# Performance work log

Measured on AMD Instinct MI355X. Metric: run time of the kernel, lower is better.

Reference implementation:

```python
import jax, jax.numpy as jnp
import numpy as np

N = 50000
E = 800000
D_IN = 256
D_HID = 256
D_OUT = 256
EPS = 1e-5


def _sage_conv(x, src, dst, Wl, Wr, b, n_nodes):
    # mean aggregation of source-node features at target nodes (PyG SAGEConv default)
    msg = x[src]                                              # [E, d_in]
    agg = jax.ops.segment_sum(msg, dst, num_segments=n_nodes)  # [N, d_in]
    deg = jax.ops.segment_sum(jnp.ones((src.shape[0],), x.dtype), dst,
                              num_segments=n_nodes)           # [N]
    agg = agg / jnp.maximum(deg, 1.0)[:, None]
    return agg @ Wl + x @ Wr + b


def _bn(h, gamma, beta, mean, var):
    # inference-mode BatchNorm1d
    return (h - mean) * jax.lax.rsqrt(var + EPS) * gamma + beta


def setup_inputs() -> dict:
    key = jax.random.key(0)
    ks = jax.random.split(key, 16)
    x = jax.random.normal(ks[0], (N, D_IN), dtype=jnp.float32)
    edge_index = jax.random.randint(ks[1], (2, E), 0, N, dtype=jnp.int32)

    def lin(k, din, dout):
        return jax.random.normal(k, (din, dout), dtype=jnp.float32) / np.sqrt(din)

    inp = {"x": x, "edge_index": edge_index}
    dims = [(D_IN, D_HID), (D_HID, D_HID), (D_HID, D_OUT)]
    ki = 2
    for i, (din, dout) in enumerate(dims):
        inp[f"Wl{i}"] = lin(ks[ki], din, dout); ki += 1
        inp[f"Wr{i}"] = lin(ks[ki], din, dout); ki += 1
        inp[f"b{i}"] = jnp.zeros((dout,), jnp.float32)
    for i in range(2):
        inp[f"gamma{i}"] = jnp.ones((D_HID,), jnp.float32)
        inp[f"beta{i}"] = jnp.zeros((D_HID,), jnp.float32)
        inp[f"mean{i}"] = jax.random.normal(ks[ki], (D_HID,), jnp.float32) * 0.1; ki += 1
        inp[f"var{i}"] = jnp.ones((D_HID,), jnp.float32) + 0.1 * jax.random.uniform(ks[ki], (D_HID,)); ki += 1
    return inp


def reference(x, edge_index, Wl0, Wr0, b0, Wl1, Wr1, b1, Wl2, Wr2, b2,
              gamma0, beta0, mean0, var0, gamma1, beta1, mean1, var1):
    src, dst = edge_index[0], edge_index[1]
    h = x
    layers = [(Wl0, Wr0, b0, gamma0, beta0, mean0, var0),
              (Wl1, Wr1, b1, gamma1, beta1, mean1, var1)]
    for Wl, Wr, b, g, bt, m, v in layers:
        h_res = h
        h = _sage_conv(h, src, dst, Wl, Wr, b, N)
        h = jax.nn.relu(_bn(h, g, bt, m, v))
        # dropout is identity in eval mode
        if h_res.shape[1] == h.shape[1]:
            h = h + h_res
    return _sage_conv(h, src, dst, Wl2, Wr2, b2, N)
```

## Files before the change

### kernel.cpp

```cpp
#include <hip/hip_runtime.h>
#include <hip/hip_bf16.h>

#define NN 50000
#define NE 800000
#define DD 256
#define EPSV 1e-5f

typedef float f32x4 __attribute__((ext_vector_type(4)));
typedef short bf16x8s __attribute__((ext_vector_type(8)));
typedef unsigned int uint32;

__device__ __forceinline__ float lo16f(uint32 u) {
  return __builtin_bit_cast(float, u << 16);
}
__device__ __forceinline__ float hi16f(uint32 u) {
  return __builtin_bit_cast(float, u & 0xffff0000u);
}
__device__ __forceinline__ float bf2f(unsigned int u16v) {
  return __builtin_bit_cast(float, u16v << 16);
}
__device__ __forceinline__ unsigned short f2bf(float f) {
  return __builtin_bit_cast(unsigned short, __float2bfloat16(f));
}
__device__ __forceinline__ void mfma_bf16(bf16x8s a, bf16x8s b, f32x4& c) {
  asm("v_mfma_f32_16x16x32_bf16 %0, %1, %2, %0" : "+v"(c) : "v"(a), "v"(b));
}
__device__ __forceinline__ void gload_lds16(const void* g, void* l) {
  __builtin_amdgcn_global_load_lds((const __attribute__((address_space(1))) void*)g,
                                   (__attribute__((address_space(3))) void*)l, 16, 0, 0);
}



__global__ void deg_count_k(const int* __restrict__ ei, int* __restrict__ deg) {
  int e = blockIdx.x * 256 + threadIdx.x;
  if (e < NE) atomicAdd(&deg[ei[NE + e]], 1);
}

__global__ void scan1_k(const int* __restrict__ deg, int* __restrict__ row_ptr,
                        int* __restrict__ blockSums) {
  __shared__ int s[1024];
  int gid = blockIdx.x * 1024 + threadIdx.x;
  int v = (gid < NN) ? deg[gid] : 0;
  s[threadIdx.x] = v;
  __syncthreads();
  for (int off = 1; off < 1024; off <<= 1) {
    int t = (threadIdx.x >= off) ? s[threadIdx.x - off] : 0;
    __syncthreads();
    s[threadIdx.x] += t;
    __syncthreads();
  }
  if (gid < NN) row_ptr[gid] = s[threadIdx.x] - v;
  if (threadIdx.x == 1023) blockSums[blockIdx.x] = s[1023];
}

__global__ void scan2_k(const int* __restrict__ blockSums, int* __restrict__ blockOffs,
                        int* __restrict__ row_ptr, int nblocks) {
  if (threadIdx.x == 0) {
    int run = 0;
    for (int i = 0; i < nblocks; ++i) { blockOffs[i] = run; run += blockSums[i]; }
    row_ptr[NN] = run;
  }
}

__global__ void scan3_k(int* __restrict__ row_ptr, const int* __restrict__ blockOffs,
                        const int* __restrict__ deg, float* __restrict__ deg_inv) {
  int gid = blockIdx.x * 1024 + threadIdx.x;
  if (gid < NN) {
    row_ptr[gid] += blockOffs[blockIdx.x];
    deg_inv[gid] = 1.0f / (float)max(deg[gid], 1);
  }
}

__global__ void csr_fill_k(const int* __restrict__ ei, int* __restrict__ cursor,
                           unsigned short* __restrict__ col16) {
  int e = blockIdx.x * 256 + threadIdx.x;
  if (e < NE) {
    int pos = atomicAdd(&cursor[ei[NE + e]], 1);
    col16[pos] = (unsigned short)ei[e];
  }
}


__global__ __launch_bounds__(256) void split_x_k(const float* __restrict__ x,
                                                 uint32* __restrict__ xc) {
  int ni = threadIdx.x & 15, c = threadIdx.x >> 4;
  int node = blockIdx.x * 16 + ni;
  const float4* xr = reinterpret_cast<const float4*>(x + (size_t)node * DD + c * 16);
  float f[16];
#pragma unroll
  for (int qq = 0; qq < 4; ++qq) {
    float4 v = xr[qq];
    f[qq * 4 + 0] = v.x; f[qq * 4 + 1] = v.y; f[qq * 4 + 2] = v.z; f[qq * 4 + 3] = v.w;
  }
  uint32 wbuf[16];
#pragma unroll
  for (int g = 0; g < 8; ++g) {
    unsigned short h0 = f2bf(f[2 * g]), h1 = f2bf(f[2 * g + 1]);
    unsigned short l0 = f2bf(f[2 * g] - bf2f(h0));
    unsigned short l1 = f2bf(f[2 * g + 1] - bf2f(h1));
    wbuf[g] = (uint32)h0 | ((uint32)h1 << 16);
    wbuf[8 + g] = (uint32)l0 | ((uint32)l1 << 16);
  }
  uint32* dst = xc + ((size_t)c * NN + node) * 16;
#pragma unroll
  for (int qq = 0; qq < 4; ++qq)
    reinterpret_cast<uint4*>(dst)[qq] =
        make_uint4(wbuf[qq * 4], wbuf[qq * 4 + 1], wbuf[qq * 4 + 2], wbuf[qq * 4 + 3]);
}


__global__ __launch_bounds__(256) void wtprep_k(
    const float* __restrict__ W0, const float* __restrict__ W1,
    const float* __restrict__ W2, const float* __restrict__ W3,
    const float* __restrict__ W4, const float* __restrict__ W5,
    unsigned short* __restrict__ wt) {
  int p = blockIdx.y;
  const float* W = (p == 0) ? W0 : (p == 1) ? W1 : (p == 2) ? W2
                   : (p == 3) ? W3 : (p == 4) ? W4 : W5;
  unsigned short* thi = wt + (size_t)(2 * p) * 65536;
  unsigned short* tlo = wt + (size_t)(2 * p + 1) * 65536;
  int gid = blockIdx.x * 256 + threadIdx.x;
  int n = gid >> 6, k4 = (gid & 63) << 2;
  ushort4 hi, lo;
  unsigned short* hp = &hi.x; unsigned short* lp = &lo.x;
#pragma unroll
  for (int r = 0; r < 4; ++r) {
    float v = W[(size_t)(k4 + r) * DD + n];
    unsigned short h = f2bf(v);
    hp[r] = h;
    lp[r] = f2bf(v - bf2f(h));
  }
  *reinterpret_cast<ushort4*>(thi + (size_t)n * DD + k4) = hi;
  *reinterpret_cast<ushort4*>(tlo + (size_t)n * DD + k4) = lo;
}


__global__ __launch_bounds__(256) void sage_agg_k(
    const uint32* __restrict__ act, const int* __restrict__ rp,
    const unsigned short* __restrict__ ci, const float* __restrict__ deg_inv,
    uint32* __restrict__ agg) {
  int b = blockIdx.x;
  int ph = (b >= 50000);
  int bb = ph ? b - 50000 : b;
  int c = ph * 8 + (bb & 7);
  int node = (bb >> 3) * 8 + (threadIdx.x >> 5);
  int t5 = threadIdx.x & 31;
  int s = t5 >> 2;
  int q = t5 & 3;

  const uint4* base = reinterpret_cast<const uint4*>(act + (size_t)c * NN * 16);
  int beg = rp[node], end = rp[node + 1];

  float a[8];
#pragma unroll
  for (int i = 0; i < 8; ++i) a[i] = 0.f;

  for (int e = beg; e < end; e += 8) {
    int ee = e + s;
    bool valid = ee < end;
    int ec = valid ? ee : beg;
    int src = (int)ci[ec];
    uint4 v = base[(size_t)src * 4 + q];
    float msk = valid ? 1.f : 0.f;
    a[0] = fmaf(msk, lo16f(v.x), a[0]); a[1] = fmaf(msk, hi16f(v.x), a[1]);
    a[2] = fmaf(msk, lo16f(v.y), a[2]); a[3] = fmaf(msk, hi16f(v.y), a[3]);
    a[4] = fmaf(msk, lo16f(v.z), a[4]); a[5] = fmaf(msk, hi16f(v.z), a[5]);
    a[6] = fmaf(msk, lo16f(v.w), a[6]); a[7] = fmaf(msk, hi16f(v.w), a[7]);
  }
#pragma unroll
  for (int i = 0; i < 8; ++i) {
    a[i] += __shfl_xor(a[i], 4);
    a[i] += __shfl_xor(a[i], 8);
    a[i] += __shfl_xor(a[i], 16);
    a[i] += __shfl_xor(a[i], 2);
  }
  float di = deg_inv[node];
#pragma unroll
  for (int i = 0; i < 8; ++i) a[i] *= di;

  uint32 wo[4];
  if (q < 2) {
#pragma unroll
    for (int i = 0; i < 4; ++i) {
      unsigned short h0 = f2bf(a[2 * i]), h1 = f2bf(a[2 * i + 1]);
      wo[i] = (uint32)h0 | ((uint32)h1 << 16);
    }
  } else {
#pragma unroll
    for (int i = 0; i < 4; ++i) {
      float t0 = a[2 * i], t1 = a[2 * i + 1];
      unsigned short l0 = f2bf(t0 - bf2f(f2bf(t0)));
      unsigned short l1 = f2bf(t1 - bf2f(f2bf(t1)));
      wo[i] = (uint32)l0 | ((uint32)l1 << 16);
    }
  }
  if (s == 0) {
    reinterpret_cast<uint4*>(agg)[((size_t)c * NN + node) * 4 + q] =
        make_uint4(wo[0], wo[1], wo[2], wo[3]);
  }
}


template <bool DO_BN>
__global__ __launch_bounds__(512) void sage_gemm_k(
    const unsigned short* __restrict__ aggC, const unsigned short* __restrict__ hC,
    const unsigned short* __restrict__ wlHi, const unsigned short* __restrict__ wlLo,
    const unsigned short* __restrict__ wrHi, const unsigned short* __restrict__ wrLo,
    const float* __restrict__ bias,
    const float* __restrict__ gamma, const float* __restrict__ beta,
    const float* __restrict__ mean, const float* __restrict__ var,
    float* __restrict__ outF, unsigned short* __restrict__ outC) {
  __shared__ __attribute__((aligned(128))) char lds[40960];

  int tid = threadIdx.x, wave = tid >> 6, l = tid & 63;
  int lr = l & 15, q = l >> 4;
  int sub = wave & 3, h = wave >> 2;
  int m0 = blockIdx.x * 64;

  f32x4 acc[8];
#pragma unroll
  for (int j = 0; j < 8; ++j) acc[j] = (f32x4)0.f;

  int rowA = m0 + lr;

#pragma unroll 1
  for (int t = 0; t < 16; ++t) {
    bool first = t < 8;
    const unsigned short* Ap = first ? aggC : hC;
    int t7 = t & 7;
#pragma unroll
    for (int i = 0; i < 5; ++i) {
      int u = wave * 5 + i;
      if (u < 8) {
        int su = u >> 1, p = u & 1;
        int row = rowA + su * 16;
        row = row < NN ? row : NN - 1;
        int c = 2 * t7 + (q >> 1);
        gload_lds16(Ap + ((size_t)c * NN + row) * 32 + p * 16 + (q & 1) * 8,
                    &lds[u * 1024 + l * 16]);
      } else {
        int ub = u - 8, j = ub >> 1, p = ub & 1;
        const unsigned short* W = first ? (p ? wlLo : wlHi) : (p ? wrLo : wrHi);
        gload_lds16(W + (size_t)(j * 16 + lr) * DD + t7 * 32 + q * 8,
                    &lds[8192 + ub * 1024 + l * 16]);
      }
    }
    __syncthreads();
    bf16x8s aH = *reinterpret_cast<const bf16x8s*>(&lds[(sub * 2 + 0) * 1024 + l * 16]);
    bf16x8s aL = *reinterpret_cast<const bf16x8s*>(&lds[(sub * 2 + 1) * 1024 + l * 16]);
#pragma unroll
    for (int jj = 0; jj < 8; ++jj) {
      int j = h * 8 + jj;
      bf16x8s bH = *reinterpret_cast<const bf16x8s*>(&lds[8192 + (j * 2 + 0) * 1024 + l * 16]);
      bf16x8s bL = *reinterpret_cast<const bf16x8s*>(&lds[8192 + (j * 2 + 1) * 1024 + l * 16]);
      mfma_bf16(aH, bH, acc[jj]);
      mfma_bf16(aH, bL, acc[jj]);
      mfma_bf16(aL, bH, acc[jj]);
    }
    __syncthreads();
  }

  if (DO_BN) {
    float* Lf = reinterpret_cast<float*>(lds);
#pragma unroll 1
    for (int g = 0; g < 4; ++g) {
      if (h == (g >> 1)) {
#pragma unroll
        for (int jj2 = 0; jj2 < 4; ++jj2) {
          int jl = (g & 1) * 4 + jj2;
          int n = (4 * g + jj2) * 16 + lr;
          float bb = bias[n];
          float sc = gamma[n] * rsqrtf(var[n] + EPSV);
          float sh = beta[n] - mean[n] * sc;
#pragma unroll
          for (int reg = 0; reg < 4; ++reg) {
            int ml = sub * 16 + 4 * q + reg;
            Lf[ml * 68 + jj2 * 16 + lr] = fmaxf((acc[jl][reg] + bb) * sc + sh, 0.f);
          }
        }
      }
      __syncthreads();
#pragma unroll
      for (int sw = 0; sw < 2; ++sw) {
        int u = (tid >> 2) + sw * 128;
        int q4 = tid & 3;
        int ml = u & 63, cc = u >> 6;
        int c = 4 * g + cc;
        int m = m0 + ml;
        if (m < NN) {
          float v[8];
          int lb = ml * 68 + cc * 16 + (q4 & 1) * 8;
#pragma unroll
          for (int i = 0; i < 8; ++i) v[i] = Lf[lb + i];
          size_t ub4 = ((size_t)c * NN + m) * 4;
          const uint4* hp = reinterpret_cast<const uint4*>(hC) + ub4;
          uint4 rh = hp[q4 & 1];
          uint4 rl = hp[2 + (q4 & 1)];
          v[0] += lo16f(rh.x) + lo16f(rl.x); v[1] += hi16f(rh.x) + hi16f(rl.x);
          v[2] += lo16f(rh.y) + lo16f(rl.y); v[3] += hi16f(rh.y) + hi16f(rl.y);
          v[4] += lo16f(rh.z) + lo16f(rl.z); v[5] += hi16f(rh.z) + hi16f(rl.z);
          v[6] += lo16f(rh.w) + lo16f(rl.w); v[7] += hi16f(rh.w) + hi16f(rl.w);
          uint32 wo[4];
          if (q4 < 2) {
#pragma unroll
            for (int i = 0; i < 4; ++i) {
              unsigned short h0 = f2bf(v[2 * i]), h1 = f2bf(v[2 * i + 1]);
              wo[i] = (uint32)h0 | ((uint32)h1 << 16);
            }
          } else {
#pragma unroll
            for (int i = 0; i < 4; ++i) {
              float t0 = v[2 * i], t1 = v[2 * i + 1];
              unsigned short l0 = f2bf(t0 - bf2f(f2bf(t0)));
              unsigned short l1 = f2bf(t1 - bf2f(f2bf(t1)));
              wo[i] = (uint32)l0 | ((uint32)l1 << 16);
            }
          }
          reinterpret_cast<uint4*>(outC)[ub4 + q4] = make_uint4(wo[0], wo[1], wo[2], wo[3]);
        }
      }
      __syncthreads();
    }
  } else {
#pragma unroll
    for (int jj = 0; jj < 8; ++jj) {
      int n = (h * 8 + jj) * 16 + lr;
      float bb = bias[n];
#pragma unroll
      for (int reg = 0; reg < 4; ++reg) {
        int m = m0 + sub * 16 + 4 * q + reg;
        if (m < NN) outF[(size_t)m * DD + n] = acc[jj][reg] + bb;
      }
    }
  }
}


extern "C" void kernel_launch(void* const* d_in, const int* in_sizes, int n_in,
                              void* d_out, int out_size, void* d_ws, size_t ws_size,
                              hipStream_t stream) {
  const float* x   = (const float*)d_in[0];
  const int*   ei  = (const int*)d_in[1];
  const float* Wl[3] = {(const float*)d_in[2], (const float*)d_in[5], (const float*)d_in[8]};
  const float* Wr[3] = {(const float*)d_in[3], (const float*)d_in[6], (const float*)d_in[9]};
  const float* bs[3] = {(const float*)d_in[4], (const float*)d_in[7], (const float*)d_in[10]};
  const float* g0  = (const float*)d_in[11];
  const float* be0 = (const float*)d_in[12];
  const float* mu0 = (const float*)d_in[13];
  const float* va0 = (const float*)d_in[14];
  const float* g1  = (const float*)d_in[15];
  const float* be1 = (const float*)d_in[16];
  const float* mu1 = (const float*)d_in[17];
  const float* va1 = (const float*)d_in[18];
  float* out = (float*)d_out;

  char* w = (char*)d_ws;
  const size_t o_deg    = 0;
  const size_t o_rowptr = 262144;
  const size_t o_cursor = 524288;
  const size_t o_col16  = 786432;
  const size_t o_deginv = 2621440;
  const size_t o_bsum   = 2883584;
  const size_t o_boff   = 2887680;
  const size_t o_wt     = 2891776;
  const size_t ACT      = (size_t)16 * NN * 64;
  const size_t o_xC     = 6291456;
  const size_t o_h1C    = o_xC + ACT;
  const size_t o_aggC   = o_xC + 2 * ACT;

  int*   deg     = (int*)(w + o_deg);
  int*   row_ptr = (int*)(w + o_rowptr);
  int*   cursor  = (int*)(w + o_cursor);
  unsigned short* col16 = (unsigned short*)(w + o_col16);
  float* deg_inv = (float*)(w + o_deginv);
  int*   bsum    = (int*)(w + o_bsum);
  int*   boff    = (int*)(w + o_boff);
  unsigned short* wt = (unsigned short*)(w + o_wt);
  uint32* xC   = (uint32*)(w + o_xC);
  uint32* h1C  = (uint32*)(w + o_h1C);
  uint32* aggC = (uint32*)(w + o_aggC);

  unsigned short* wlT[3][2];
  unsigned short* wrT[3][2];
  for (int l = 0; l < 3; ++l) {
    wlT[l][0] = wt + (size_t)(4 * l + 0) * 65536;
    wlT[l][1] = wt + (size_t)(4 * l + 1) * 65536;
    wrT[l][0] = wt + (size_t)(4 * l + 2) * 65536;
    wrT[l][1] = wt + (size_t)(4 * l + 3) * 65536;
  }

  const int SCAN_BLOCKS = (NN + 1023) / 1024;

  hipMemsetAsync(deg, 0, NN * sizeof(int), stream);
  deg_count_k<<<NE / 256, 256, 0, stream>>>(ei, deg);
  scan1_k<<<SCAN_BLOCKS, 1024, 0, stream>>>(deg, row_ptr, bsum);
  scan2_k<<<1, 64, 0, stream>>>(bsum, boff, row_ptr, SCAN_BLOCKS);
  scan3_k<<<SCAN_BLOCKS, 1024, 0, stream>>>(row_ptr, boff, deg, deg_inv);
  hipMemcpyAsync(cursor, row_ptr, NN * sizeof(int), hipMemcpyDeviceToDevice, stream);
  csr_fill_k<<<NE / 256, 256, 0, stream>>>(ei, cursor, col16);

  split_x_k<<<NN / 16, 256, 0, stream>>>(x, xC);
  wtprep_k<<<dim3(64, 6), 256, 0, stream>>>(Wl[0], Wr[0], Wl[1], Wr[1], Wl[2], Wr[2], wt);

  const int AGRID = 100000;
  dim3 ggrid((NN + 63) / 64);

  sage_agg_k<<<AGRID, 256, 0, stream>>>(xC, row_ptr, col16, deg_inv, aggC);
  sage_gemm_k<true><<<ggrid, 512, 0, stream>>>(
      (const unsigned short*)aggC, (const unsigned short*)xC,
      wlT[0][0], wlT[0][1], wrT[0][0], wrT[0][1],
      bs[0], g0, be0, mu0, va0, nullptr, (unsigned short*)h1C);
  sage_agg_k<<<AGRID, 256, 0, stream>>>(h1C, row_ptr, col16, deg_inv, aggC);
  sage_gemm_k<true><<<ggrid, 512, 0, stream>>>(
      (const unsigned short*)aggC, (const unsigned short*)h1C,
      wlT[1][0], wlT[1][1], wrT[1][0], wrT[1][1],
      bs[1], g1, be1, mu1, va1, nullptr, (unsigned short*)xC);
  sage_agg_k<<<AGRID, 256, 0, stream>>>(xC, row_ptr, col16, deg_inv, aggC);
  sage_gemm_k<false><<<ggrid, 512, 0, stream>>>(
      (const unsigned short*)aggC, (const unsigned short*)xC,
      wlT[2][0], wlT[2][1], wrT[2][0], wrT[2][1],
      bs[2], nullptr, nullptr, nullptr, nullptr, out, nullptr);
}
```

Measured before the change: 936.8 us.

## Store activations as chunked fp32 and split to bf16 hi/lo inside GEMM

Intermediate activations were stored as pre-split bf16 hi/lo pairs in a chunked layout. They are now stored as plain fp32 in 16-column chunks, and the hi/lo split happens in registers after the LDS load in the GEMM. The aggregation kernel is rewritten so four threads per node each accumulate a float4 over edges, with no cross-lane shuffle reduction. The GEMM epilogue writes BN+ReLU+residual directly without an LDS staging pass, and the prep kernels and cursor memcpy are merged into fewer launches. The activation bytes are the same, but the epilogue stores become strided scalar writes and the split arithmetic moves into the GEMM inner loop.

```diff
diff --git a/kernel.cpp b/kernel.cpp
--- a/kernel.cpp
+++ b/kernel.cpp
@@ -9,13 +9,8 @@
 typedef float f32x4 __attribute__((ext_vector_type(4)));
 typedef short bf16x8s __attribute__((ext_vector_type(8)));
 typedef unsigned int uint32;
-
-__device__ __forceinline__ float lo16f(uint32 u) {
-  return __builtin_bit_cast(float, u << 16);
-}
-__device__ __forceinline__ float hi16f(uint32 u) {
-  return __builtin_bit_cast(float, u & 0xffff0000u);
-}
+typedef uint32 u32x4 __attribute__((ext_vector_type(4)));
+
 __device__ __forceinline__ float bf2f(unsigned int u16v) {
   return __builtin_bit_cast(float, u16v << 16);
 }
@@ -64,10 +59,13 @@
 }
 
 __global__ void scan3_k(int* __restrict__ row_ptr, const int* __restrict__ blockOffs,
-                        const int* __restrict__ deg, float* __restrict__ deg_inv) {
+                        const int* __restrict__ deg, float* __restrict__ deg_inv,
+                        int* __restrict__ cursor) {
   int gid = blockIdx.x * 1024 + threadIdx.x;
   if (gid < NN) {
-    row_ptr[gid] += blockOffs[blockIdx.x];
+    int v = row_ptr[gid] + blockOffs[blockIdx.x];
+    row_ptr[gid] = v;
+    cursor[gid] = v;
     deg_inv[gid] = 1.0f / (float)max(deg[gid], 1);
   }
 }
@@ -82,173 +80,135 @@
 }
 
 
-__global__ __launch_bounds__(256) void split_x_k(const float* __restrict__ x,
-                                                 uint32* __restrict__ xc) {
-  int ni = threadIdx.x & 15, c = threadIdx.x >> 4;
-  int node = blockIdx.x * 16 + ni;
-  const float4* xr = reinterpret_cast<const float4*>(x + (size_t)node * DD + c * 16);
-  float f[16];
-#pragma unroll
-  for (int qq = 0; qq < 4; ++qq) {
-    float4 v = xr[qq];
-    f[qq * 4 + 0] = v.x; f[qq * 4 + 1] = v.y; f[qq * 4 + 2] = v.z; f[qq * 4 + 3] = v.w;
-  }
-  uint32 wbuf[16];
-#pragma unroll
-  for (int g = 0; g < 8; ++g) {
-    unsigned short h0 = f2bf(f[2 * g]), h1 = f2bf(f[2 * g + 1]);
-    unsigned short l0 = f2bf(f[2 * g] - bf2f(h0));
-    unsigned short l1 = f2bf(f[2 * g + 1] - bf2f(h1));
-    wbuf[g] = (uint32)h0 | ((uint32)h1 << 16);
-    wbuf[8 + g] = (uint32)l0 | ((uint32)l1 << 16);
-  }
-  uint32* dst = xc + ((size_t)c * NN + node) * 16;
-#pragma unroll
-  for (int qq = 0; qq < 4; ++qq)
-    reinterpret_cast<uint4*>(dst)[qq] =
-        make_uint4(wbuf[qq * 4], wbuf[qq * 4 + 1], wbuf[qq * 4 + 2], wbuf[qq * 4 + 3]);
-}
-
-
-__global__ __launch_bounds__(256) void wtprep_k(
+__global__ __launch_bounds__(256) void prep_k(
+    const float* __restrict__ x,
     const float* __restrict__ W0, const float* __restrict__ W1,
     const float* __restrict__ W2, const float* __restrict__ W3,
     const float* __restrict__ W4, const float* __restrict__ W5,
-    unsigned short* __restrict__ wt) {
-  int p = blockIdx.y;
-  const float* W = (p == 0) ? W0 : (p == 1) ? W1 : (p == 2) ? W2
-                   : (p == 3) ? W3 : (p == 4) ? W4 : W5;
-  unsigned short* thi = wt + (size_t)(2 * p) * 65536;
-  unsigned short* tlo = wt + (size_t)(2 * p + 1) * 65536;
-  int gid = blockIdx.x * 256 + threadIdx.x;
-  int n = gid >> 6, k4 = (gid & 63) << 2;
-  ushort4 hi, lo;
-  unsigned short* hp = &hi.x; unsigned short* lp = &lo.x;
-#pragma unroll
-  for (int r = 0; r < 4; ++r) {
-    float v = W[(size_t)(k4 + r) * DD + n];
-    unsigned short h = f2bf(v);
-    hp[r] = h;
-    lp[r] = f2bf(v - bf2f(h));
-  }
-  *reinterpret_cast<ushort4*>(thi + (size_t)n * DD + k4) = hi;
-  *reinterpret_cast<ushort4*>(tlo + (size_t)n * DD + k4) = lo;
+    float* __restrict__ xF, unsigned short* __restrict__ wt) {
+  if (blockIdx.x < 3125) {
+    int unit = blockIdx.x * 256 + threadIdx.x;
+    int c = unit / NN, node = unit - c * NN;
+    const float4* src = reinterpret_cast<const float4*>(x + (size_t)node * DD + c * 16);
+    float4* dst = reinterpret_cast<float4*>(xF + (size_t)unit * 16);
+#pragma unroll
+    for (int i = 0; i < 4; ++i) dst[i] = src[i];
+  } else {
+    int bb = blockIdx.x - 3125;
+    int p = bb >> 6;
+    const float* W = (p == 0) ? W0 : (p == 1) ? W1 : (p == 2) ? W2
+                     : (p == 3) ? W3 : (p == 4) ? W4 : W5;
+    unsigned short* thi = wt + (size_t)(2 * p) * 65536;
+    unsigned short* tlo = wt + (size_t)(2 * p + 1) * 65536;
+    int gid = (bb & 63) * 256 + threadIdx.x;
+    int n = gid >> 6, k4 = (gid & 63) << 2;
+    ushort4 hi, lo;
+    unsigned short* hp = &hi.x; unsigned short* lp = &lo.x;
+#pragma unroll
+    for (int r = 0; r < 4; ++r) {
+      float v = W[(size_t)(k4 + r) * DD + n];
+      unsigned short h = f2bf(v);
+      hp[r] = h;
+      lp[r] = f2bf(v - bf2f(h));
+    }
+    *reinterpret_cast<ushort4*>(thi + (size_t)n * DD + k4) = hi;
+    *reinterpret_cast<ushort4*>(tlo + (size_t)n * DD + k4) = lo;
+  }
 }
 
 
 __global__ __launch_bounds__(256) void sage_agg_k(
-    const uint32* __restrict__ act, const int* __restrict__ rp,
+    const float* __restrict__ act, const int* __restrict__ rp,
     const unsigned short* __restrict__ ci, const float* __restrict__ deg_inv,
-    uint32* __restrict__ agg) {
+    float* __restrict__ agg) {
   int b = blockIdx.x;
-  int ph = (b >= 50000);
-  int bb = ph ? b - 50000 : b;
+  int ph = (b >= 6256);
+  int bb = ph ? b - 6256 : b;
   int c = ph * 8 + (bb & 7);
-  int node = (bb >> 3) * 8 + (threadIdx.x >> 5);
-  int t5 = threadIdx.x & 31;
-  int s = t5 >> 2;
-  int q = t5 & 3;
-
-  const uint4* base = reinterpret_cast<const uint4*>(act + (size_t)c * NN * 16);
+  int grp = bb >> 3;
+  int node = grp * 64 + (threadIdx.x >> 2);
+  if (node >= NN) return;
+  int q4 = (threadIdx.x & 3) * 4;
+
+  const float* base = act + (size_t)c * NN * 16;
   int beg = rp[node], end = rp[node + 1];
 
-  float a[8];
-#pragma unroll
-  for (int i = 0; i < 8; ++i) a[i] = 0.f;
-
-  for (int e = beg; e < end; e += 8) {
-    int ee = e + s;
-    bool valid = ee < end;
-    int ec = valid ? ee : beg;
-    int src = (int)ci[ec];
-    uint4 v = base[(size_t)src * 4 + q];
-    float msk = valid ? 1.f : 0.f;
-    a[0] = fmaf(msk, lo16f(v.x), a[0]); a[1] = fmaf(msk, hi16f(v.x), a[1]);
-    a[2] = fmaf(msk, lo16f(v.y), a[2]); a[3] = fmaf(msk, hi16f(v.y), a[3]);
-    a[4] = fmaf(msk, lo16f(v.z), a[4]); a[5] = fmaf(msk, hi16f(v.z), a[5]);
-    a[6] = fmaf(msk, lo16f(v.w), a[6]); a[7] = fmaf(msk, hi16f(v.w), a[7]);
-  }
-#pragma unroll
-  for (int i = 0; i < 8; ++i) {
-    a[i] += __shfl_xor(a[i], 4);
-    a[i] += __shfl_xor(a[i], 8);
-    a[i] += __shfl_xor(a[i], 16);
-    a[i] += __shfl_xor(a[i], 2);
-  }
+  f32x4 a0 = (f32x4)0.f, a1 = (f32x4)0.f;
+  int e = beg;
+  for (; e + 2 <= end; e += 2) {
+    int s0 = (int)ci[e], s1 = (int)ci[e + 1];
+    f32x4 v0 = *reinterpret_cast<const f32x4*>(base + (size_t)s0 * 16 + q4);
+    f32x4 v1 = *reinterpret_cast<const f32x4*>(base + (size_t)s1 * 16 + q4);
+    a0 += v0;
+    a1 += v1;
+  }
+  if (e < end)
+    a0 += *reinterpret_cast<const f32x4*>(base + (size_t)ci[e] * 16 + q4);
+  a0 += a1;
   float di = deg_inv[node];
-#pragma unroll
-  for (int i = 0; i < 8; ++i) a[i] *= di;
-
-  uint32 wo[4];
-  if (q < 2) {
-#pragma unroll
-    for (int i = 0; i < 4; ++i) {
-      unsigned short h0 = f2bf(a[2 * i]), h1 = f2bf(a[2 * i + 1]);
-      wo[i] = (uint32)h0 | ((uint32)h1 << 16);
-    }
-  } else {
-#pragma unroll
-    for (int i = 0; i < 4; ++i) {
-      float t0 = a[2 * i], t1 = a[2 * i + 1];
-      unsigned short l0 = f2bf(t0 - bf2f(f2bf(t0)));
-      unsigned short l1 = f2bf(t1 - bf2f(f2bf(t1)));
-      wo[i] = (uint32)l0 | ((uint32)l1 << 16);
-    }
-  }
-  if (s == 0) {
-    reinterpret_cast<uint4*>(agg)[((size_t)c * NN + node) * 4 + q] =
-        make_uint4(wo[0], wo[1], wo[2], wo[3]);
-  }
+  a0 *= di;
+  *reinterpret_cast<f32x4*>(agg + ((size_t)c * NN + node) * 16 + q4) = a0;
 }
 
 
 template <bool DO_BN>
 __global__ __launch_bounds__(512) void sage_gemm_k(
-    const unsigned short* __restrict__ aggC, const unsigned short* __restrict__ hC,
+    const float* __restrict__ aggF, const float* __restrict__ hF,
     const unsigned short* __restrict__ wlHi, const unsigned short* __restrict__ wlLo,
     const unsigned short* __restrict__ wrHi, const unsigned short* __restrict__ wrLo,
     const float* __restrict__ bias,
     const float* __restrict__ gamma, const float* __restrict__ beta,
     const float* __restrict__ mean, const float* __restrict__ var,
-    float* __restrict__ outF, unsigned short* __restrict__ outC) {
+    float* __restrict__ outF, float* __restrict__ outC) {
   __shared__ __attribute__((aligned(128))) char lds[40960];
 
   int tid = threadIdx.x, wave = tid >> 6, l = tid & 63;
-  int lr = l & 15, q = l >> 4;
+  int lr = l & 15, lq = l >> 4;
   int sub = wave & 3, h = wave >> 2;
   int m0 = blockIdx.x * 64;
 
   f32x4 acc[8];
 #pragma unroll
   for (int j = 0; j < 8; ++j) acc[j] = (f32x4)0.f;
-
-  int rowA = m0 + lr;
 
 #pragma unroll 1
   for (int t = 0; t < 16; ++t) {
     bool first = t < 8;
-    const unsigned short* Ap = first ? aggC : hC;
+    const float* Ap = first ? aggF : hF;
     int t7 = t & 7;
 #pragma unroll
     for (int i = 0; i < 5; ++i) {
       int u = wave * 5 + i;
       if (u < 8) {
-        int su = u >> 1, p = u & 1;
-        int row = rowA + su * 16;
+        int row = m0 + (u & 3) * 16 + (l & 15);
         row = row < NN ? row : NN - 1;
-        int c = 2 * t7 + (q >> 1);
-        gload_lds16(Ap + ((size_t)c * NN + row) * 32 + p * 16 + (q & 1) * 8,
+        gload_lds16(Ap + ((size_t)(2 * t7 + (u >> 2)) * NN + row) * 16 + (l >> 4) * 4,
                     &lds[u * 1024 + l * 16]);
       } else {
         int ub = u - 8, j = ub >> 1, p = ub & 1;
         const unsigned short* W = first ? (p ? wlLo : wlHi) : (p ? wrLo : wrHi);
-        gload_lds16(W + (size_t)(j * 16 + lr) * DD + t7 * 32 + q * 8,
+        gload_lds16(W + (size_t)(j * 16 + (l & 15)) * DD + t7 * 32 + (l >> 4) * 8,
                     &lds[8192 + ub * 1024 + l * 16]);
       }
     }
     __syncthreads();
-    bf16x8s aH = *reinterpret_cast<const bf16x8s*>(&lds[(sub * 2 + 0) * 1024 + l * 16]);
-    bf16x8s aL = *reinterpret_cast<const bf16x8s*>(&lds[(sub * 2 + 1) * 1024 + l * 16]);
+    int ua = (lq >> 1) * 4 + sub;
+    int abase = ua * 1024 + (lq & 1) * 512 + lr * 16;
+    f32x4 f0 = *reinterpret_cast<const f32x4*>(&lds[abase]);
+    f32x4 f1 = *reinterpret_cast<const f32x4*>(&lds[abase + 256]);
+    float af[8] = {f0[0], f0[1], f0[2], f0[3], f1[0], f1[1], f1[2], f1[3]};
+    u32x4 hw, lw;
+#pragma unroll
+    for (int i = 0; i < 4; ++i) {
+      uint32 b0 = __builtin_bit_cast(uint32, af[2 * i]);
+      uint32 b1 = __builtin_bit_cast(uint32, af[2 * i + 1]);
+      hw[i] = (b1 & 0xffff0000u) | (b0 >> 16);
+      float l0 = af[2 * i] - __builtin_bit_cast(float, b0 & 0xffff0000u);
+      float l1 = af[2 * i + 1] - __builtin_bit_cast(float, b1 & 0xffff0000u);
+      lw[i] = (uint32)f2bf(l0) | ((uint32)f2bf(l1) << 16);
+    }
+    bf16x8s aH = __builtin_bit_cast(bf16x8s, hw);
+    bf16x8s aL = __builtin_bit_cast(bf16x8s, lw);
 #pragma unroll
     for (int jj = 0; jj < 8; ++jj) {
       int j = h * 8 + jj;
@@ -261,76 +221,28 @@
     __syncthreads();
   }
 
-  if (DO_BN) {
-    float* Lf = reinterpret_cast<float*>(lds);
-#pragma unroll 1
-    for (int g = 0; g < 4; ++g) {
-      if (h == (g >> 1)) {
-#pragma unroll
-        for (int jj2 = 0; jj2 < 4; ++jj2) {
-          int jl = (g & 1) * 4 + jj2;
-          int n = (4 * g + jj2) * 16 + lr;
-          float bb = bias[n];
-          float sc = gamma[n] * rsqrtf(var[n] + EPSV);
-          float sh = beta[n] - mean[n] * sc;
-#pragma unroll
-          for (int reg = 0; reg < 4; ++reg) {
-            int ml = sub * 16 + 4 * q + reg;
-            Lf[ml * 68 + jj2 * 16 + lr] = fmaxf((acc[jl][reg] + bb) * sc + sh, 0.f);
-          }
+#pragma unroll
+  for (int jj = 0; jj < 8; ++jj) {
+    int cj = h * 8 + jj;
+    int n = cj * 16 + lr;
+    float bb = bias[n], sc = 0.f, sh = 0.f;
+    if (DO_BN) {
+      float s = gamma[n] * rsqrtf(var[n] + EPSV);
+      sc = s;
+      sh = beta[n] - mean[n] * s;
+    }
+#pragma unroll
+    for (int reg = 0; reg < 4; ++reg) {
+      int m = m0 + sub * 16 + lq * 4 + reg;
+      if (m < NN) {
+        float v = acc[jj][reg] + bb;
+        if (DO_BN) {
+          size_t ui = ((size_t)cj * NN + m) * 16 + lr;
+          v = fmaxf(v * sc + sh, 0.f) + hF[ui];
+          outC[ui] = v;
+        } else {
+          outF[(size_t)m * DD + n] = v;
         }
-      }
-      __syncthreads();
-#pragma unroll
-      for (int sw = 0; sw < 2; ++sw) {
-        int u = (tid >> 2) + sw * 128;
-        int q4 = tid & 3;
-        int ml = u & 63, cc = u >> 6;
-        int c = 4 * g + cc;
-        int m = m0 + ml;
-        if (m < NN) {
-          float v[8];
-          int lb = ml * 68 + cc * 16 + (q4 & 1) * 8;
-#pragma unroll
-          for (int i = 0; i < 8; ++i) v[i] = Lf[lb + i];
-          size_t ub4 = ((size_t)c * NN + m) * 4;
-          const uint4* hp = reinterpret_cast<const uint4*>(hC) + ub4;
-          uint4 rh = hp[q4 & 1];
-          uint4 rl = hp[2 + (q4 & 1)];
-          v[0] += lo16f(rh.x) + lo16f(rl.x); v[1] += hi16f(rh.x) + hi16f(rl.x);
-          v[2] += lo16f(rh.y) + lo16f(rl.y); v[3] += hi16f(rh.y) + hi16f(rl.y);
-          v[4] += lo16f(rh.z) + lo16f(rl.z); v[5] += hi16f(rh.z) + hi16f(rl.z);
-          v[6] += lo16f(rh.w) + lo16f(rl.w); v[7] += hi16f(rh.w) + hi16f(rl.w);
-          uint32 wo[4];
-          if (q4 < 2) {
-#pragma unroll
-            for (int i = 0; i < 4; ++i) {
-              unsigned short h0 = f2bf(v[2 * i]), h1 = f2bf(v[2 * i + 1]);
-              wo[i] = (uint32)h0 | ((uint32)h1 << 16);
-            }
-          } else {
-#pragma unroll
-            for (int i = 0; i < 4; ++i) {
-              float t0 = v[2 * i], t1 = v[2 * i + 1];
-              unsigned short l0 = f2bf(t0 - bf2f(f2bf(t0)));
-              unsigned short l1 = f2bf(t1 - bf2f(f2bf(t1)));
-              wo[i] = (uint32)l0 | ((uint32)l1 << 16);
-            }
-          }
-          reinterpret_cast<uint4*>(outC)[ub4 + q4] = make_uint4(wo[0], wo[1], wo[2], wo[3]);
-        }
-      }
-      __syncthreads();
-    }
-  } else {
-#pragma unroll
-    for (int jj = 0; jj < 8; ++jj) {
-      int n = (h * 8 + jj) * 16 + lr;
-      float bb = bias[n];
-#pragma unroll
-      for (int reg = 0; reg < 4; ++reg) {
-        int m = m0 + sub * 16 + 4 * q + reg;
-        if (m < NN) outF[(size_t)m * DD + n] = acc[jj][reg] + bb;
       }
     }
   }
@@ -365,9 +277,9 @@
   const size_t o_boff   = 2887680;
   const size_t o_wt     = 2891776;
   const size_t ACT      = (size_t)16 * NN * 64;
-  const size_t o_xC     = 6291456;
-  const size_t o_h1C    = o_xC + ACT;
-  const size_t o_aggC   = o_xC + 2 * ACT;
+  const size_t o_xF     = 6291456;
+  const size_t o_h1F    = o_xF + ACT;
+  const size_t o_aggF   = o_xF + 2 * ACT;
 
   int*   deg     = (int*)(w + o_deg);
   int*   row_ptr = (int*)(w + o_rowptr);
@@ -377,9 +289,9 @@
   int*   bsum    = (int*)(w + o_bsum);
   int*   boff    = (int*)(w + o_boff);
   unsigned short* wt = (unsigned short*)(w + o_wt);
-  uint32* xC   = (uint32*)(w + o_xC);
-  uint32* h1C  = (uint32*)(w + o_h1C);
-  uint32* aggC = (uint32*)(w + o_aggC);
+  float* xF   = (float*)(w + o_xF);
+  float* h1F  = (float*)(w + o_h1F);
+  float* aggF = (float*)(w + o_aggF);
 
   unsigned short* wlT[3][2];
   unsigned short* wrT[3][2];
@@ -396,29 +308,24 @@
   deg_count_k<<<NE / 256, 256, 0, stream>>>(ei, deg);
   scan1_k<<<SCAN_BLOCKS, 1024, 0, stream>>>(deg, row_ptr, bsum);
   scan2_k<<<1, 64, 0, stream>>>(bsum, boff, row_ptr, SCAN_BLOCKS);
-  scan3_k<<<SCAN_BLOCKS, 1024, 0, stream>>>(row_ptr, boff, deg, deg_inv);
-  hipMemcpyAsync(cursor, row_ptr, NN * sizeof(int), hipMemcpyDeviceToDevice, stream);
+  scan3_k<<<SCAN_BLOCKS, 1024, 0, stream>>>(row_ptr, boff, deg, deg_inv, cursor);
   csr_fill_k<<<NE / 256, 256, 0, stream>>>(ei, cursor, col16);
 
-  split_x_k<<<NN / 16, 256, 0, stream>>>(x, xC);
-  wtprep_k<<<dim3(64, 6), 256, 0, stream>>>(Wl[0], Wr[0], Wl[1], Wr[1], Wl[2], Wr[2], wt);
-
-  const int AGRID = 100000;
+  prep_k<<<3509, 256, 0, stream>>>(x, Wl[0], Wr[0], Wl[1], Wr[1], Wl[2], Wr[2], xF, wt);
+
+  const int AGRID = 12512;
   dim3 ggrid((NN + 63) / 64);
 
-  sage_agg_k<<<AGRID, 256, 0, stream>>>(xC, row_ptr, col16, deg_inv, aggC);
+  sage_agg_k<<<AGRID, 256, 0, stream>>>(xF, row_ptr, col16, deg_inv, aggF);
   sage_gemm_k<true><<<ggrid, 512, 0, stream>>>(
-      (const unsigned short*)aggC, (const unsigned short*)xC,
-      wlT[0][0], wlT[0][1], wrT[0][0], wrT[0][1],
-      bs[0], g0, be0, mu0, va0, nullptr, (unsigned short*)h1C);
-  sage_agg_k<<<AGRID, 256, 0, stream>>>(h1C, row_ptr, col16, deg_inv, aggC);
+      aggF, xF, wlT[0][0], wlT[0][1], wrT[0][0], wrT[0][1],
+      bs[0], g0, be0, mu0, va0, nullptr, h1F);
+  sage_agg_k<<<AGRID, 256, 0, stream>>>(h1F, row_ptr, col16, deg_inv, aggF);
   sage_gemm_k<true><<<ggrid, 512, 0, stream>>>(
-      (const unsigned short*)aggC, (const unsigned short*)h1C,
-      wlT[1][0], wlT[1][1], wrT[1][0], wrT[1][1],
-      bs[1], g1, be1, mu1, va1, nullptr, (unsigned short*)xC);
-  sage_agg_k<<<AGRID, 256, 0, stream>>>(xC, row_ptr, col16, deg_inv, aggC);
+      aggF, h1F, wlT[1][0], wlT[1][1], wrT[1][0], wrT[1][1],
+      bs[1], g1, be1, mu1, va1, nullptr, xF);
+  sage_agg_k<<<AGRID, 256, 0, stream>>>(xF, row_ptr, col16, deg_inv, aggF);
   sage_gemm_k<false><<<ggrid, 512, 0, stream>>>(
-      (const unsigned short*)aggC, (const unsigned short*)xC,
-      wlT[2][0], wlT[2][1], wrT[2][0], wrT[2][1],
+      aggF, xF, wlT[2][0], wlT[2][1], wrT[2][0], wrT[2][1],
       bs[2], nullptr, nullptr, nullptr, nullptr, out, nullptr);
 }
```

Measured after the change: 749.5 us. 1.25x faster.
